# Kernel optimization log

Hardware: AMD Instinct MI355X
Metric: run time of the kernel (lower is better)

## Reference

```python
import jax, jax.numpy as jnp
import numpy as np

N = 80000      # points
H = 32         # neighbors per point
K = 15         # kernel points (torch-points3d default)
CIN = 128
COUT = 256
D2 = COUT // 4  # 64
INFL = 0.4      # point_influence = prev_grid_size * sigma
KP_RADIUS = 1.5 * INFL  # torch-points3d kernel radius
EPS = 1e-5
SLOPE = 0.2


def setup_inputs() -> dict:
    key = jax.random.key(0)
    ks = jax.random.split(key, 12)
    feats = jax.random.normal(ks[0], (N, CIN), jnp.float32)
    xyz = jax.random.uniform(ks[1], (N, 3), dtype=jnp.float32)
    batch = jnp.zeros((N,), jnp.int32)
    neighbor_idx = jax.random.randint(ks[2], (N, H), 0, N)
    # unary_1: Linear(CIN, D2, bias=False) + BN params
    W1 = jax.random.normal(ks[3], (CIN, D2), jnp.float32) / np.float32(np.sqrt(CIN))
    g1 = jnp.ones((D2,), jnp.float32); b1 = jnp.zeros((D2,), jnp.float32)
    # fixed kernel points inside ball of radius KP_RADIUS (buffer, not trained)
    kdir = jax.random.normal(ks[4], (K, 3), jnp.float32)
    kdir = kdir / jnp.linalg.norm(kdir, axis=1, keepdims=True)
    kp_points = kdir * jax.random.uniform(ks[5], (K, 1), dtype=jnp.float32) * KP_RADIUS
    # per-kernel-point weight matrices [K, D2, D2]
    kp_weights = jax.random.normal(ks[6], (K, D2, D2), jnp.float32) / np.float32(np.sqrt(K * D2))
    # unary_2: Linear(D2, COUT, bias=False) + BN params
    W2 = jax.random.normal(ks[7], (D2, COUT), jnp.float32) / np.float32(np.sqrt(D2))
    g2 = jnp.ones((COUT,), jnp.float32); b2 = jnp.zeros((COUT,), jnp.float32)
    # shortcut: Linear(CIN, COUT, bias=False) + BN params
    Wsc = jax.random.normal(ks[8], (CIN, COUT), jnp.float32) / np.float32(np.sqrt(CIN))
    gsc = jnp.ones((COUT,), jnp.float32); bsc = jnp.zeros((COUT,), jnp.float32)
    return {"feats": feats, "xyz": xyz, "batch": batch, "neighbor_idx": neighbor_idx,
            "W1": W1, "g1": g1, "b1": b1, "kp_points": kp_points, "kp_weights": kp_weights,
            "W2": W2, "g2": g2, "b2": b2, "Wsc": Wsc, "gsc": gsc, "bsc": bsc}


def _bn(x, g, b):
    # FastBatchNorm1d training-mode forward on [N, C]: biased batch stats
    m = jnp.mean(x, axis=0)
    v = jnp.var(x, axis=0)
    return (x - m) * jax.lax.rsqrt(v + EPS) * g + b


def _act(x):
    return jax.nn.leaky_relu(x, SLOPE)


def reference(feats, xyz, batch, neighbor_idx, W1, g1, b1, kp_points, kp_weights,
              W2, g2, b2, Wsc, gsc, bsc):
    # unary_1
    x = _act(_bn(feats @ W1, g1, b1))              # [N, D2]
    # KPConv: gather neighbors, kernel-point linear influence, weighted aggregation
    neighbors = xyz[neighbor_idx] - xyz[:, None, :]            # [N, H, 3]
    diff = neighbors[:, :, None, :] - kp_points[None, None]    # [N, H, K, 3]
    sq = jnp.sum(diff * diff, axis=-1)                          # [N, H, K]
    w = jnp.maximum(1.0 - jnp.sqrt(sq) / INFL, 0.0)             # linear influence
    nx = x[neighbor_idx]                                        # [N, H, D2]
    fk = jnp.einsum('nhk,nhd->nkd', w, nx)                      # [N, K, D2]
    x = jnp.einsum('nkd,kde->ne', fk, kp_weights)               # [N, D2]
    # unary_2
    x = _act(_bn(x @ W2, g2, b2))                               # [N, COUT]
    # shortcut (in_channels != out_channels -> Linear + BN)
    shortcut = _bn(feats @ Wsc, gsc, bsc)                       # [N, COUT]
    return x + shortcut
```

## Files before the change

kernel.cpp:

```cpp
#include <hip/hip_runtime.h>
#include <math.h>

#define NPTS 80000
#define NBH 32
#define KP 15
#define CIN 128
#define COUT 256
#define D2 64
#define INFL 0.4f
#define EPS 1e-5f
#define SLOPE 0.2f

typedef __attribute__((ext_vector_type(8))) short short8;
typedef __attribute__((ext_vector_type(4))) float f32x4;

__device__ inline ushort f2b(float x) {
  unsigned u = __float_as_uint(x);
  return (ushort)((u + 0x7FFFu + ((u >> 16) & 1u)) >> 16);
}
__device__ inline float b2f(ushort v) { return __uint_as_float(((unsigned)v) << 16); }

__global__ __launch_bounds__(256) void k_prep(const float* __restrict__ feats,
                                              const float* __restrict__ W1,
                                              const float* __restrict__ W2,
                                              const float* __restrict__ Wsc,
                                              const float* __restrict__ kw,
                                              ushort* __restrict__ featsb,
                                              ushort* __restrict__ w1s,
                                              ushort* __restrict__ w2s,
                                              ushort* __restrict__ wscs,
                                              ushort* __restrict__ kws) {
  const int NF4 = NPTS * CIN / 4;
  const int TOT = NF4 + 118784;
  int stride = gridDim.x * 256;
  for (int i = blockIdx.x * 256 + threadIdx.x; i < TOT; i += stride) {
    if (i < NF4) {
      float4 v = reinterpret_cast<const float4*>(feats)[i];
      ushort4 o;
      o.x = f2b(v.x); o.y = f2b(v.y); o.z = f2b(v.z); o.w = f2b(v.w);
      reinterpret_cast<ushort4*>(featsb)[i] = o;
    } else {
      int j = i - NF4;
      const float* src;
      ushort* dst;
      int logN;
      if (j < 8192)       { src = W1;  dst = w1s;  logN = 6; }
      else if (j < 24576) { j -= 8192;  src = W2;  dst = w2s;  logN = 8; }
      else if (j < 57344) { j -= 24576; src = Wsc; dst = wscs; logN = 8; }
      else                { j -= 57344; src = kw;  dst = kws;  logN = 6; }
      int N = 1 << logN, NT = N >> 4;
      int k = j >> logN, n = j & (N - 1);
      int dsti = ((k >> 5) * NT + (n >> 4)) * 512 + (n & 15) * 32 + ((k >> 3) & 3) * 8 + (k & 7);
      dst[dsti] = f2b(src[j]);
    }
  }
}

template <int NCOLS>
__global__ __launch_bounds__(256) void k_gemm_mfma(const ushort* __restrict__ A,
                                                   const ushort* __restrict__ Bsw,
                                                   ushort* __restrict__ Cb, int K) {
  constexpr int NT = NCOLS / 16;
  int tid = threadIdx.x;
  int wave = tid >> 6, lane = tid & 63;
  int nn = lane & 15, q = lane >> 4;
  int row0 = blockIdx.x * 64 + wave * 16;
  f32x4 acc[NT];
#pragma unroll
  for (int c = 0; c < NT; ++c) acc[c] = (f32x4){0.f, 0.f, 0.f, 0.f};
  const ushort* ap = A + (size_t)(row0 + nn) * K + q * 8;
  int nch = K >> 5;
  for (int ch = 0; ch < nch; ++ch) {
    short8 af = *reinterpret_cast<const short8*>(ap + (size_t)ch * 32);
    const ushort* bp = Bsw + (size_t)ch * NT * 512 + nn * 32 + q * 8;
#pragma unroll
    for (int c = 0; c < NT; ++c) {
      short8 bf = *reinterpret_cast<const short8*>(bp + c * 512);
      acc[c] = __builtin_amdgcn_mfma_f32_16x16x32_bf16(af, bf, acc[c], 0, 0, 0);
    }
  }
#pragma unroll
  for (int c = 0; c < NT; ++c)
#pragma unroll
    for (int r = 0; r < 4; ++r)
      Cb[(size_t)(row0 + q * 4 + r) * NCOLS + c * 16 + nn] = f2b(acc[c][r]);
}

__global__ __launch_bounds__(256) void k_colstats_b16(const ushort* __restrict__ X, int units,
                                                      int cols, float* __restrict__ sum,
                                                      float* __restrict__ sumsq) {
  __shared__ float ls[2048], ls2[2048];
  int tid = threadIdx.x;
  int stride = gridDim.x * 256;
  float s[8], s2[8];
#pragma unroll
  for (int k = 0; k < 8; ++k) { s[k] = 0.f; s2[k] = 0.f; }
  for (int i = blockIdx.x * 256 + tid; i < units; i += stride) {
    short8 v = reinterpret_cast<const short8*>(X)[i];
#pragma unroll
    for (int k = 0; k < 8; ++k) {
      float f = b2f((ushort)v[k]);
      s[k] += f;
      s2[k] += f * f;
    }
  }
#pragma unroll
  for (int k = 0; k < 8; ++k) { ls[tid * 8 + k] = s[k]; ls2[tid * 8 + k] = s2[k]; }
  __syncthreads();
  if (tid < cols) {
    int P = cols >> 3;
    float a = 0.f, a2 = 0.f;
    for (int t = (tid >> 3); t < 256; t += P) {
      a += ls[t * 8 + (tid & 7)];
      a2 += ls2[t * 8 + (tid & 7)];
    }
    atomicAdd(&sum[tid], a);
    atomicAdd(&sumsq[tid], a2);
  }
}

__global__ __launch_bounds__(256) void k_normb(const ushort* __restrict__ X,
                                               const float* __restrict__ sum,
                                               const float* __restrict__ sumsq,
                                               const float* __restrict__ g,
                                               const float* __restrict__ b,
                                               ushort* __restrict__ out) {
  __shared__ float sc[64], sh[64];
  int tid = threadIdx.x;
  if (tid < 64) {
    float m = sum[tid] * (1.0f / NPTS);
    float v = sumsq[tid] * (1.0f / NPTS) - m * m;
    float s = g[tid] * rsqrtf(v + EPS);
    sc[tid] = s;
    sh[tid] = b[tid] - m * s;
  }
  __syncthreads();
  const int units = NPTS * 8;
  int stride = gridDim.x * 256;
  for (int i = blockIdx.x * 256 + tid; i < units; i += stride) {
    short8 v = reinterpret_cast<const short8*>(X)[i];
    int cb = (i & 7) * 8;
    short8 o;
#pragma unroll
    for (int k = 0; k < 8; ++k) {
      float a = b2f((ushort)v[k]) * sc[cb + k] + sh[cb + k];
      a = a > 0.f ? a : SLOPE * a;
      o[k] = (short)f2b(a);
    }
    reinterpret_cast<short8*>(out)[i] = o;
  }
}

__global__ __launch_bounds__(256, 3) void k_kpfused(const ushort* __restrict__ X1b,
                                                    const float* __restrict__ xyz,
                                                    const int* __restrict__ nidx,
                                                    const float* __restrict__ kpp,
                                                    const ushort* __restrict__ kws,
                                                    const ushort* __restrict__ w2s,
                                                    ushort* __restrict__ Y3b) {
  __shared__ ushort s_xT[4][64][32];
  __shared__ ushort s_fk[30 * 512];
  __shared__ ushort s_y2[2 * 512];
  int tid = threadIdx.x;
  int w = tid >> 6, lane = tid & 63;
  int q = lane >> 4, nn = lane & 15;
  int l8 = lane >> 3, c8 = lane & 7;
  int n_base = blockIdx.x * 16;

  int kidx = nn < 15 ? nn : 0;
  float kpx = kpp[kidx * 3 + 0], kpy = kpp[kidx * 3 + 1], kpz = kpp[kidx * 3 + 2];

  int nb[4];
  float rx[4], ry[4], rz[4];
#pragma unroll
  for (int p = 0; p < 4; ++p) {
    int n = n_base + w * 4 + p;
    nb[p] = 0; rx[p] = 0.f; ry[p] = 0.f; rz[p] = 0.f;
    if (lane < 32) {
      int t = nidx[n * NBH + lane];
      nb[p] = t;
      rx[p] = xyz[t * 3 + 0] - xyz[n * 3 + 0];
      ry[p] = xyz[t * 3 + 1] - xyz[n * 3 + 1];
      rz[p] = xyz[t * 3 + 2] - xyz[n * 3 + 2];
    }
  }
  short8 g[4][4];
#pragma unroll
  for (int p = 0; p < 4; ++p)
#pragma unroll
    for (int it = 0; it < 4; ++it) {
      int nbh = __shfl(nb[p], it * 8 + l8);
      g[p][it] = *reinterpret_cast<const short8*>(X1b + (size_t)nbh * 64 + c8 * 8);
    }

#pragma unroll
  for (int p = 0; p < 4; ++p) {
    short8 af;
#pragma unroll
    for (int j = 0; j < 8; ++j) {
      int hh = q * 8 + j;
      float dx = __shfl(rx[p], hh) - kpx;
      float dy = __shfl(ry[p], hh) - kpy;
      float dz = __shfl(rz[p], hh) - kpz;
      float dist = sqrtf(dx * dx + dy * dy + dz * dz);
      float wv = fmaxf(1.0f - dist * (1.0f / INFL), 0.0f);
      if (nn == 15) wv = 0.f;
      af[j] = (short)f2b(wv);
    }
#pragma unroll
    for (int it = 0; it < 4; ++it) {
      int hh = it * 8 + l8;
      int hcol = hh ^ ((c8 & 3) << 3);
#pragma unroll
      for (int u = 0; u < 8; ++u) s_xT[w][c8 * 8 + u][hcol] = (ushort)g[p][it][u];
    }
    f32x4 acc[4];
#pragma unroll
    for (int c = 0; c < 4; ++c) {
      int d = c * 16 + nn;
      int key = (d >> 3) & 3;
      short8 bf = *reinterpret_cast<const short8*>(&s_xT[w][d][(q ^ key) << 3]);
      acc[c] = __builtin_amdgcn_mfma_f32_16x16x32_bf16(af, bf, (f32x4){0.f, 0.f, 0.f, 0.f}, 0, 0, 0);
    }
    int m = w * 4 + p;
#pragma unroll
    for (int c = 0; c < 4; ++c) {
#pragma unroll
      for (int r = 0; r < 4; ++r) {
        int kpt = q * 4 + r;
        if (kpt < 15) {
          int kap = kpt * 64 + c * 16 + nn;
          int ch = kap >> 5, t = kap & 31;
          int tp = t ^ (((ch >> 3) & 3) << 3);
          s_fk[ch * 512 + m * 32 + tp] = f2b(acc[c][r]);
        }
      }
    }
  }
  __syncthreads();

  f32x4 acc2 = (f32x4){0.f, 0.f, 0.f, 0.f};
  for (int ch = 0; ch < 30; ++ch) {
    int key = (ch >> 3) & 3;
    short8 a = *reinterpret_cast<const short8*>(&s_fk[ch * 512 + nn * 32 + ((q ^ key) << 3)]);
    short8 b = *reinterpret_cast<const short8*>(kws + (size_t)ch * 2048 + w * 512 + nn * 32 + q * 8);
    acc2 = __builtin_amdgcn_mfma_f32_16x16x32_bf16(a, b, acc2, 0, 0, 0);
  }
  {
    int e = w * 16 + nn;
    int ch2 = e >> 5, t = e & 31;
#pragma unroll
    for (int r = 0; r < 4; ++r) {
      int mm = q * 4 + r;
      int tp = t ^ (((mm >> 2) & 3) << 3);
      s_y2[ch2 * 512 + mm * 32 + tp] = f2b(acc2[r]);
    }
  }
  __syncthreads();

  short8 a0, a1;
  {
    int key = (nn >> 2) & 3;
    a0 = *reinterpret_cast<const short8*>(&s_y2[0 * 512 + nn * 32 + ((q ^ key) << 3)]);
    a1 = *reinterpret_cast<const short8*>(&s_y2[1 * 512 + nn * 32 + ((q ^ key) << 3)]);
  }
#pragma unroll
  for (int t4 = 0; t4 < 4; ++t4) {
    int ct = w * 4 + t4;
    short8 b0 = *reinterpret_cast<const short8*>(w2s + (0 * 16 + ct) * 512 + nn * 32 + q * 8);
    short8 b1 = *reinterpret_cast<const short8*>(w2s + (1 * 16 + ct) * 512 + nn * 32 + q * 8);
    f32x4 a = __builtin_amdgcn_mfma_f32_16x16x32_bf16(a0, b0, (f32x4){0.f, 0.f, 0.f, 0.f}, 0, 0, 0);
    a = __builtin_amdgcn_mfma_f32_16x16x32_bf16(a1, b1, a, 0, 0, 0);
#pragma unroll
    for (int r = 0; r < 4; ++r)
      Y3b[(size_t)(n_base + q * 4 + r) * 256 + ct * 16 + nn] = f2b(a[r]);
  }
}

__global__ __launch_bounds__(256) void k_final(const ushort* __restrict__ Y3,
                                               const ushort* __restrict__ YSC,
                                               const float* __restrict__ s3,
                                               const float* __restrict__ ss3,
                                               const float* __restrict__ g2,
                                               const float* __restrict__ b2,
                                               const float* __restrict__ ssc,
                                               const float* __restrict__ sssc,
                                               const float* __restrict__ gsc,
                                               const float* __restrict__ bsc,
                                               float* __restrict__ out) {
  __shared__ float sc3[256], sh3[256], scc[256], shc[256];
  int tid = threadIdx.x;
  {
    float m = s3[tid] * (1.0f / NPTS);
    float v = ss3[tid] * (1.0f / NPTS) - m * m;
    float s = g2[tid] * rsqrtf(v + EPS);
    sc3[tid] = s;
    sh3[tid] = b2[tid] - m * s;
    m = ssc[tid] * (1.0f / NPTS);
    v = sssc[tid] * (1.0f / NPTS) - m * m;
    s = gsc[tid] * rsqrtf(v + EPS);
    scc[tid] = s;
    shc[tid] = bsc[tid] - m * s;
  }
  __syncthreads();
  const int units = NPTS * 32;
  int stride = gridDim.x * 256;
  for (int i = blockIdx.x * 256 + tid; i < units; i += stride) {
    short8 a = reinterpret_cast<const short8*>(Y3)[i];
    short8 b = reinterpret_cast<const short8*>(YSC)[i];
    int cb = (i & 31) * 8;
    float o[8];
#pragma unroll
    for (int k = 0; k < 8; ++k) {
      float x = b2f((ushort)a[k]) * sc3[cb + k] + sh3[cb + k];
      x = x > 0.f ? x : SLOPE * x;
      o[k] = x + b2f((ushort)b[k]) * scc[cb + k] + shc[cb + k];
    }
    float4* O4 = reinterpret_cast<float4*>(out + (size_t)i * 8);
    O4[0] = make_float4(o[0], o[1], o[2], o[3]);
    O4[1] = make_float4(o[4], o[5], o[6], o[7]);
  }
}

extern "C" void kernel_launch(void* const* d_in, const int* in_sizes, int n_in,
                              void* d_out, int out_size, void* d_ws, size_t ws_size,
                              hipStream_t stream) {
  const float* feats = (const float*)d_in[0];
  const float* xyz   = (const float*)d_in[1];
  const int* nidx    = (const int*)d_in[3];
  const float* W1    = (const float*)d_in[4];
  const float* g1    = (const float*)d_in[5];
  const float* b1    = (const float*)d_in[6];
  const float* kpp   = (const float*)d_in[7];
  const float* kw    = (const float*)d_in[8];
  const float* W2    = (const float*)d_in[9];
  const float* g2    = (const float*)d_in[10];
  const float* b2    = (const float*)d_in[11];
  const float* Wsc   = (const float*)d_in[12];
  const float* gsc   = (const float*)d_in[13];
  const float* bsc   = (const float*)d_in[14];
  float* out = (float*)d_out;

  char* ws = (char*)d_ws;
  ushort* featsb = (ushort*)ws;
  ushort* X1r    = (ushort*)(ws + 20480000);
  ushort* X1b    = (ushort*)(ws + 30720000);
  ushort* Y3b    = (ushort*)(ws + 40960000);
  ushort* YSCb   = (ushort*)(ws + 81920000);
  ushort* w1s    = (ushort*)(ws + 122880000);
  ushort* w2s    = w1s + 8192;
  ushort* wscs   = w2s + 16384;
  ushort* kws    = wscs + 32768;
  float*  ST     = (float*)(kws + 61440);
  float *S1 = ST, *SS1 = ST + 64;
  float *S3 = ST + 128, *SS3 = ST + 384;
  float *SSC = ST + 640, *SSSC = ST + 896;

  hipMemsetAsync(ST, 0, 1152 * sizeof(float), stream);
  k_prep<<<2048, 256, 0, stream>>>(feats, W1, W2, Wsc, kw, featsb, w1s, w2s, wscs, kws);
  k_gemm_mfma<64><<<1250, 256, 0, stream>>>(featsb, w1s, X1r, 128);
  k_colstats_b16<<<256, 256, 0, stream>>>(X1r, NPTS * 8, 64, S1, SS1);
  k_normb<<<512, 256, 0, stream>>>(X1r, S1, SS1, g1, b1, X1b);
  k_gemm_mfma<256><<<1250, 256, 0, stream>>>(featsb, wscs, YSCb, 128);
  k_colstats_b16<<<256, 256, 0, stream>>>(YSCb, NPTS * 32, 256, SSC, SSSC);
  k_kpfused<<<NPTS / 16, 256, 0, stream>>>(X1b, xyz, nidx, kpp, kws, w2s, Y3b);
  k_colstats_b16<<<256, 256, 0, stream>>>(Y3b, NPTS * 32, 256, S3, SS3);
  k_final<<<1024, 256, 0, stream>>>(Y3b, YSCb, S3, SS3, g2, b2, SSC, SSSC, gsc, bsc, out);
}
```

Measured before the change: 380.7 us.

## Fuse both input GEMMs and fold BN column stats into GEMM epilogues

Merges the W1 and shortcut GEMMs into one kernel so the feature tile is read once. Computes per-column sum and sum-of-squares in the GEMM and KPConv epilogues with wave shuffles and global atomics, which removes the three separate colstats passes that re-read the bf16 intermediates. The cost is many more global atomics on a few hundred addresses (per wave, per column tile) and higher register pressure from holding 20 accumulator tiles.

Result: slower. 527.5 us (+38.6%).

```diff
diff --git a/kernel.cpp b/kernel.cpp
--- a/kernel.cpp
+++ b/kernel.cpp
@@ -56,66 +56,74 @@
   }
 }
 
-template <int NCOLS>
-__global__ __launch_bounds__(256) void k_gemm_mfma(const ushort* __restrict__ A,
-                                                   const ushort* __restrict__ Bsw,
-                                                   ushort* __restrict__ Cb, int K) {
-  constexpr int NT = NCOLS / 16;
+__global__ __launch_bounds__(256) void k_gemm_dual(const ushort* __restrict__ A,
+                                                   const ushort* __restrict__ w1s,
+                                                   const ushort* __restrict__ wscs,
+                                                   ushort* __restrict__ X1r,
+                                                   ushort* __restrict__ YSCb,
+                                                   float* __restrict__ S1,
+                                                   float* __restrict__ SS1,
+                                                   float* __restrict__ SSC,
+                                                   float* __restrict__ SSSC) {
   int tid = threadIdx.x;
   int wave = tid >> 6, lane = tid & 63;
   int nn = lane & 15, q = lane >> 4;
   int row0 = blockIdx.x * 64 + wave * 16;
-  f32x4 acc[NT];
-#pragma unroll
-  for (int c = 0; c < NT; ++c) acc[c] = (f32x4){0.f, 0.f, 0.f, 0.f};
-  const ushort* ap = A + (size_t)(row0 + nn) * K + q * 8;
-  int nch = K >> 5;
-  for (int ch = 0; ch < nch; ++ch) {
-    short8 af = *reinterpret_cast<const short8*>(ap + (size_t)ch * 32);
-    const ushort* bp = Bsw + (size_t)ch * NT * 512 + nn * 32 + q * 8;
-#pragma unroll
-    for (int c = 0; c < NT; ++c) {
-      short8 bf = *reinterpret_cast<const short8*>(bp + c * 512);
-      acc[c] = __builtin_amdgcn_mfma_f32_16x16x32_bf16(af, bf, acc[c], 0, 0, 0);
-    }
-  }
-#pragma unroll
-  for (int c = 0; c < NT; ++c)
-#pragma unroll
-    for (int r = 0; r < 4; ++r)
-      Cb[(size_t)(row0 + q * 4 + r) * NCOLS + c * 16 + nn] = f2b(acc[c][r]);
-}
-
-__global__ __launch_bounds__(256) void k_colstats_b16(const ushort* __restrict__ X, int units,
-                                                      int cols, float* __restrict__ sum,
-                                                      float* __restrict__ sumsq) {
-  __shared__ float ls[2048], ls2[2048];
-  int tid = threadIdx.x;
-  int stride = gridDim.x * 256;
-  float s[8], s2[8];
-#pragma unroll
-  for (int k = 0; k < 8; ++k) { s[k] = 0.f; s2[k] = 0.f; }
-  for (int i = blockIdx.x * 256 + tid; i < units; i += stride) {
-    short8 v = reinterpret_cast<const short8*>(X)[i];
-#pragma unroll
-    for (int k = 0; k < 8; ++k) {
-      float f = b2f((ushort)v[k]);
-      s[k] += f;
-      s2[k] += f * f;
-    }
-  }
-#pragma unroll
-  for (int k = 0; k < 8; ++k) { ls[tid * 8 + k] = s[k]; ls2[tid * 8 + k] = s2[k]; }
-  __syncthreads();
-  if (tid < cols) {
-    int P = cols >> 3;
-    float a = 0.f, a2 = 0.f;
-    for (int t = (tid >> 3); t < 256; t += P) {
-      a += ls[t * 8 + (tid & 7)];
-      a2 += ls2[t * 8 + (tid & 7)];
-    }
-    atomicAdd(&sum[tid], a);
-    atomicAdd(&sumsq[tid], a2);
+  f32x4 acc1[4], acc2[16];
+#pragma unroll
+  for (int c = 0; c < 4; ++c) acc1[c] = (f32x4){0.f, 0.f, 0.f, 0.f};
+#pragma unroll
+  for (int c = 0; c < 16; ++c) acc2[c] = (f32x4){0.f, 0.f, 0.f, 0.f};
+  const ushort* ap = A + (size_t)(row0 + nn) * CIN + q * 8;
+#pragma unroll
+  for (int ch = 0; ch < 4; ++ch) {
+    short8 af = *reinterpret_cast<const short8*>(ap + ch * 32);
+    const ushort* bp1 = w1s + (size_t)ch * 4 * 512 + nn * 32 + q * 8;
+    const ushort* bp2 = wscs + (size_t)ch * 16 * 512 + nn * 32 + q * 8;
+#pragma unroll
+    for (int c = 0; c < 4; ++c) {
+      short8 bf = *reinterpret_cast<const short8*>(bp1 + c * 512);
+      acc1[c] = __builtin_amdgcn_mfma_f32_16x16x32_bf16(af, bf, acc1[c], 0, 0, 0);
+    }
+#pragma unroll
+    for (int c = 0; c < 16; ++c) {
+      short8 bf = *reinterpret_cast<const short8*>(bp2 + c * 512);
+      acc2[c] = __builtin_amdgcn_mfma_f32_16x16x32_bf16(af, bf, acc2[c], 0, 0, 0);
+    }
+  }
+#pragma unroll
+  for (int c = 0; c < 4; ++c) {
+    float s = 0.f, s2 = 0.f;
+#pragma unroll
+    for (int r = 0; r < 4; ++r) {
+      ushort o = f2b(acc1[c][r]);
+      X1r[(size_t)(row0 + q * 4 + r) * D2 + c * 16 + nn] = o;
+      float v = b2f(o);
+      s += v; s2 += v * v;
+    }
+    s += __shfl_xor(s, 16); s += __shfl_xor(s, 32);
+    s2 += __shfl_xor(s2, 16); s2 += __shfl_xor(s2, 32);
+    if (q == 0) {
+      atomicAdd(&S1[c * 16 + nn], s);
+      atomicAdd(&SS1[c * 16 + nn], s2);
+    }
+  }
+#pragma unroll
+  for (int c = 0; c < 16; ++c) {
+    float s = 0.f, s2 = 0.f;
+#pragma unroll
+    for (int r = 0; r < 4; ++r) {
+      ushort o = f2b(acc2[c][r]);
+      YSCb[(size_t)(row0 + q * 4 + r) * COUT + c * 16 + nn] = o;
+      float v = b2f(o);
+      s += v; s2 += v * v;
+    }
+    s += __shfl_xor(s, 16); s += __shfl_xor(s, 32);
+    s2 += __shfl_xor(s2, 16); s2 += __shfl_xor(s2, 32);
+    if (q == 0) {
+      atomicAdd(&SSC[c * 16 + nn], s);
+      atomicAdd(&SSSC[c * 16 + nn], s2);
+    }
   }
 }
 
@@ -157,7 +165,9 @@
                                                     const float* __restrict__ kpp,
                                                     const ushort* __restrict__ kws,
                                                     const ushort* __restrict__ w2s,
-                                                    ushort* __restrict__ Y3b) {
+                                                    ushort* __restrict__ Y3b,
+                                                    float* __restrict__ S3,
+                                                    float* __restrict__ SS3) {
   __shared__ ushort s_xT[4][64][32];
   __shared__ ushort s_fk[30 * 512];
   __shared__ ushort s_y2[2 * 512];
@@ -271,9 +281,20 @@
     short8 b1 = *reinterpret_cast<const short8*>(w2s + (1 * 16 + ct) * 512 + nn * 32 + q * 8);
     f32x4 a = __builtin_amdgcn_mfma_f32_16x16x32_bf16(a0, b0, (f32x4){0.f, 0.f, 0.f, 0.f}, 0, 0, 0);
     a = __builtin_amdgcn_mfma_f32_16x16x32_bf16(a1, b1, a, 0, 0, 0);
-#pragma unroll
-    for (int r = 0; r < 4; ++r)
-      Y3b[(size_t)(n_base + q * 4 + r) * 256 + ct * 16 + nn] = f2b(a[r]);
+    float s = 0.f, s2 = 0.f;
+#pragma unroll
+    for (int r = 0; r < 4; ++r) {
+      ushort o = f2b(a[r]);
+      Y3b[(size_t)(n_base + q * 4 + r) * 256 + ct * 16 + nn] = o;
+      float v = b2f(o);
+      s += v; s2 += v * v;
+    }
+    s += __shfl_xor(s, 16); s += __shfl_xor(s, 32);
+    s2 += __shfl_xor(s2, 16); s2 += __shfl_xor(s2, 32);
+    if (q == 0) {
+      atomicAdd(&S3[ct * 16 + nn], s);
+      atomicAdd(&SS3[ct * 16 + nn], s2);
+    }
   }
 }
 
@@ -358,12 +379,8 @@
 
   hipMemsetAsync(ST, 0, 1152 * sizeof(float), stream);
   k_prep<<<2048, 256, 0, stream>>>(feats, W1, W2, Wsc, kw, featsb, w1s, w2s, wscs, kws);
-  k_gemm_mfma<64><<<1250, 256, 0, stream>>>(featsb, w1s, X1r, 128);
-  k_colstats_b16<<<256, 256, 0, stream>>>(X1r, NPTS * 8, 64, S1, SS1);
+  k_gemm_dual<<<1250, 256, 0, stream>>>(featsb, w1s, wscs, X1r, YSCb, S1, SS1, SSC, SSSC);
   k_normb<<<512, 256, 0, stream>>>(X1r, S1, SS1, g1, b1, X1b);
-  k_gemm_mfma<256><<<1250, 256, 0, stream>>>(featsb, wscs, YSCb, 128);
-  k_colstats_b16<<<256, 256, 0, stream>>>(YSCb, NPTS * 32, 256, SSC, SSSC);
-  k_kpfused<<<NPTS / 16, 256, 0, stream>>>(X1b, xyz, nidx, kpp, kws, w2s, Y3b);
-  k_colstats_b16<<<256, 256, 0, stream>>>(Y3b, NPTS * 32, 256, S3, SS3);
+  k_kpfused<<<NPTS / 16, 256, 0, stream>>>(X1b, xyz, nidx, kpp, kws, w2s, Y3b, S3, SS3);
   k_final<<<1024, 256, 0, stream>>>(Y3b, YSCb, S3, SS3, g2, b2, SSC, SSSC, gsc, bsc, out);
 }
```
